# Kernel optimization log

Hardware: AMD Instinct MI355X
Metric: run time of the kernel (lower is better)

## Reference

```python
import jax, jax.numpy as jnp
import numpy as np

N = 2_000_000  # number of poses
EPS_THETA = 1e-6  # small-angle threshold from original module


def setup_inputs() -> dict:
    key = jax.random.key(0)
    k1, k2 = jax.random.split(key)
    xi = jax.random.normal(k1, (N, 6), dtype=jnp.float32) * 0.1  # (n,6) lie-algebra params
    poses_init = jax.random.normal(k2, (N, 4, 4), dtype=jnp.float32)  # (n,4,4) initial poses
    return {"xi": xi, "poses_init": poses_init}


def _skew(v):
    # v: (n,3) -> (n,3,3) skew-symmetric matrices
    z = jnp.zeros_like(v[..., 0])
    return jnp.stack([
        jnp.stack([z, -v[..., 2], v[..., 1]], axis=-1),
        jnp.stack([v[..., 2], z, -v[..., 0]], axis=-1),
        jnp.stack([-v[..., 1], v[..., 0], z], axis=-1),
    ], axis=-2)


def reference(xi, poses_init):
    # xi: (n,6) = [translation t (3), rotation omega (3)]
    t = xi[:, :3]
    omega = xi[:, 3:]
    theta = jnp.linalg.norm(omega, axis=-1)            # (n,)
    small = theta < EPS_THETA
    safe_theta = jnp.where(small, jnp.ones_like(theta), theta)
    k = omega / safe_theta[:, None]                    # unit axis
    K = _skew(k)                                       # (n,3,3)
    I3 = jnp.eye(3, dtype=xi.dtype)
    s = jnp.sin(theta)[:, None, None]
    c = (1.0 - jnp.cos(theta))[:, None, None]
    R_rod = I3 + s * K + c * jnp.einsum('nij,njk->nik', K, K)
    R_small = I3 + _skew(omega)                        # first-order branch as in original
    R = jnp.where(small[:, None, None], R_small, R_rod)  # (n,3,3)

    # assemble (n,4,4) homogeneous transform [[R, t], [0, 1]]
    top = jnp.concatenate([R, t[:, :, None]], axis=-1)               # (n,3,4)
    bottom_row = jnp.array([0.0, 0.0, 0.0, 1.0], dtype=xi.dtype)
    bottom = jnp.broadcast_to(bottom_row, (xi.shape[0], 1, 4))
    T = jnp.concatenate([top, bottom], axis=1)                       # (n,4,4)

    # right-multiply by initial poses: delta @ pose_init
    return jnp.einsum('nij,njk->nik', T, poses_init)
```

## Files before the change

### kernel.cpp

```cpp
#include <hip/hip_runtime.h>
#include <hip/hip_bf16.h>

#define EPS_THETA 1e-6f

__global__ __launch_bounds__(256) void se3_compose_kernel(
    const float* __restrict__ xi,
    const float* __restrict__ poses,
    float* __restrict__ out,
    int n)
{
    int i = blockIdx.x * blockDim.x + threadIdx.x;
    if (i >= n) return;

    const float2* x2 = (const float2*)(xi + 6ll * i);
    float2 a = x2[0];
    float2 b = x2[1];
    float2 c2 = x2[2];
    float t0 = a.x, t1 = a.y, t2 = b.x;
    float w0 = b.y, w1 = c2.x, w2 = c2.y;

    float theta2 = w0 * w0 + w1 * w1 + w2 * w2;
    float theta  = sqrtf(theta2);
    bool  small_ = theta < EPS_THETA;

    float inv = small_ ? 1.0f : (1.0f / theta);
    float k0 = w0 * inv, k1 = w1 * inv, k2 = w2 * inv;

    float s = small_ ? 1.0f : sinf(theta);
    float c = small_ ? 0.0f : (1.0f - cosf(theta));

    float R00 = 1.0f + c * (k0 * k0 - 1.0f);
    float R01 = c * k0 * k1 - s * k2;
    float R02 = c * k0 * k2 + s * k1;
    float R10 = c * k0 * k1 + s * k2;
    float R11 = 1.0f + c * (k1 * k1 - 1.0f);
    float R12 = c * k1 * k2 - s * k0;
    float R20 = c * k0 * k2 - s * k1;
    float R21 = c * k1 * k2 + s * k0;
    float R22 = 1.0f + c * (k2 * k2 - 1.0f);

    const float4* P = (const float4*)(poses + 16ll * i);
    float4 p0 = P[0];
    float4 p1 = P[1];
    float4 p2 = P[2];
    float4 p3 = P[3];

    float4* O = (float4*)(out + 16ll * i);

    float4 o0, o1, o2;
    o0.x = R00 * p0.x + R01 * p1.x + R02 * p2.x + t0 * p3.x;
    o0.y = R00 * p0.y + R01 * p1.y + R02 * p2.y + t0 * p3.y;
    o0.z = R00 * p0.z + R01 * p1.z + R02 * p2.z + t0 * p3.z;
    o0.w = R00 * p0.w + R01 * p1.w + R02 * p2.w + t0 * p3.w;

    o1.x = R10 * p0.x + R11 * p1.x + R12 * p2.x + t1 * p3.x;
    o1.y = R10 * p0.y + R11 * p1.y + R12 * p2.y + t1 * p3.y;
    o1.z = R10 * p0.z + R11 * p1.z + R12 * p2.z + t1 * p3.z;
    o1.w = R10 * p0.w + R11 * p1.w + R12 * p2.w + t1 * p3.w;

    o2.x = R20 * p0.x + R21 * p1.x + R22 * p2.x + t2 * p3.x;
    o2.y = R20 * p0.y + R21 * p1.y + R22 * p2.y + t2 * p3.y;
    o2.z = R20 * p0.z + R21 * p1.z + R22 * p2.z + t2 * p3.z;
    o2.w = R20 * p0.w + R21 * p1.w + R22 * p2.w + t2 * p3.w;

    O[0] = o0;
    O[1] = o1;
    O[2] = o2;
    O[3] = p3;
}

extern "C" void kernel_launch(void* const* d_in, const int* in_sizes, int n_in,
                              void* d_out, int out_size, void* d_ws, size_t ws_size,
                              hipStream_t stream) {
    const float* xi    = (const float*)d_in[0];
    const float* poses = (const float*)d_in[1];
    float*       out   = (float*)d_out;

    int n = in_sizes[0] / 6;

    const int block = 256;
    const int grid  = (n + block - 1) / block;
    se3_compose_kernel<<<grid, block, 0, stream>>>(xi, poses, out, n);
}
```

Measured before the change: 256.8 us.

## Split each pose across four lanes for coalesced float4 loads and stores

```diff
diff --git a/kernel.cpp b/kernel.cpp
--- a/kernel.cpp
+++ b/kernel.cpp
@@ -3,21 +3,35 @@
 
 #define EPS_THETA 1e-6f
 
+__device__ __forceinline__ float4 shfl4(float4 v, int src) {
+    float4 r;
+    r.x = __shfl(v.x, src, 4);
+    r.y = __shfl(v.y, src, 4);
+    r.z = __shfl(v.z, src, 4);
+    r.w = __shfl(v.w, src, 4);
+    return r;
+}
+
 __global__ __launch_bounds__(256) void se3_compose_kernel(
     const float* __restrict__ xi,
-    const float* __restrict__ poses,
-    float* __restrict__ out,
-    int n)
+    const float4* __restrict__ poses4,
+    float4* __restrict__ out4,
+    int n4)
 {
     int i = blockIdx.x * blockDim.x + threadIdx.x;
-    if (i >= n) return;
+    if (i >= n4) return;
 
-    const float2* x2 = (const float2*)(xi + 6ll * i);
-    float2 a = x2[0];
-    float2 b = x2[1];
-    float2 c2 = x2[2];
+    int p = i >> 2;
+    int r = i & 3;
+
+    const float2* x2 = (const float2*)(xi + 6ll * p);
+    float2 a  = x2[0];
+    float2 b  = x2[1];
+    float2 cc = x2[2];
     float t0 = a.x, t1 = a.y, t2 = b.x;
-    float w0 = b.y, w1 = c2.x, w2 = c2.y;
+    float w0 = b.y, w1 = cc.x, w2 = cc.y;
+
+    float4 pr = poses4[i];
 
     float theta2 = w0 * w0 + w1 * w1 + w2 * w2;
     float theta  = sqrtf(theta2);
@@ -39,46 +53,36 @@
     float R21 = c * k1 * k2 + s * k0;
     float R22 = 1.0f + c * (k2 * k2 - 1.0f);
 
-    const float4* P = (const float4*)(poses + 16ll * i);
-    float4 p0 = P[0];
-    float4 p1 = P[1];
-    float4 p2 = P[2];
-    float4 p3 = P[3];
+    float c0 = (r == 0) ? R00 : (r == 1) ? R10 : (r == 2) ? R20 : 0.0f;
+    float c1 = (r == 0) ? R01 : (r == 1) ? R11 : (r == 2) ? R21 : 0.0f;
+    float c2 = (r == 0) ? R02 : (r == 1) ? R12 : (r == 2) ? R22 : 0.0f;
+    float c3 = (r == 0) ? t0  : (r == 1) ? t1  : (r == 2) ? t2  : 1.0f;
 
-    float4* O = (float4*)(out + 16ll * i);
+    float4 P0 = shfl4(pr, 0);
+    float4 P1 = shfl4(pr, 1);
+    float4 P2 = shfl4(pr, 2);
+    float4 P3 = shfl4(pr, 3);
 
-    float4 o0, o1, o2;
-    o0.x = R00 * p0.x + R01 * p1.x + R02 * p2.x + t0 * p3.x;
-    o0.y = R00 * p0.y + R01 * p1.y + R02 * p2.y + t0 * p3.y;
-    o0.z = R00 * p0.z + R01 * p1.z + R02 * p2.z + t0 * p3.z;
-    o0.w = R00 * p0.w + R01 * p1.w + R02 * p2.w + t0 * p3.w;
+    float4 o;
+    o.x = c0 * P0.x + c1 * P1.x + c2 * P2.x + c3 * P3.x;
+    o.y = c0 * P0.y + c1 * P1.y + c2 * P2.y + c3 * P3.y;
+    o.z = c0 * P0.z + c1 * P1.z + c2 * P2.z + c3 * P3.z;
+    o.w = c0 * P0.w + c1 * P1.w + c2 * P2.w + c3 * P3.w;
 
-    o1.x = R10 * p0.x + R11 * p1.x + R12 * p2.x + t1 * p3.x;
-    o1.y = R10 * p0.y + R11 * p1.y + R12 * p2.y + t1 * p3.y;
-    o1.z = R10 * p0.z + R11 * p1.z + R12 * p2.z + t1 * p3.z;
-    o1.w = R10 * p0.w + R11 * p1.w + R12 * p2.w + t1 * p3.w;
-
-    o2.x = R20 * p0.x + R21 * p1.x + R22 * p2.x + t2 * p3.x;
-    o2.y = R20 * p0.y + R21 * p1.y + R22 * p2.y + t2 * p3.y;
-    o2.z = R20 * p0.z + R21 * p1.z + R22 * p2.z + t2 * p3.z;
-    o2.w = R20 * p0.w + R21 * p1.w + R22 * p2.w + t2 * p3.w;
-
-    O[0] = o0;
-    O[1] = o1;
-    O[2] = o2;
-    O[3] = p3;
+    out4[i] = o;
 }
 
 extern "C" void kernel_launch(void* const* d_in, const int* in_sizes, int n_in,
                               void* d_out, int out_size, void* d_ws, size_t ws_size,
                               hipStream_t stream) {
-    const float* xi    = (const float*)d_in[0];
-    const float* poses = (const float*)d_in[1];
-    float*       out   = (float*)d_out;
+    const float*  xi     = (const float*)d_in[0];
+    const float4* poses4 = (const float4*)d_in[1];
+    float4*       out4   = (float4*)d_out;
 
-    int n = in_sizes[0] / 6;
+    int n  = in_sizes[0] / 6;
+    int n4 = 4 * n;
 
     const int block = 256;
-    const int grid  = (n + block - 1) / block;
-    se3_compose_kernel<<<grid, block, 0, stream>>>(xi, poses, out, n);
+    const int grid  = (n4 + block - 1) / block;
+    se3_compose_kernel<<<grid, block, 0, stream>>>(xi, poses4, out4, n4);
 }
```

Result: faster. 246.3 us (-4.1%).
